# Optimization experiments

Hardware: AMD Instinct MI355X
Metric: run time of the kernel (lower is better)

The kernel has to match this reference:

```python
import jax, jax.numpy as jnp
import numpy as np

N = 1024
NODE_DIM = 3
HIDDEN = 128
NLAYERS = 3
HEADS = 4
HD = HIDDEN // HEADS  # 32
EPS = 1e-5
NEG = -1e9


def setup_inputs() -> dict:
    key = jax.random.key(0)
    ks = jax.random.split(key, 32)
    def w(k, shape, fan_in):
        return jax.random.normal(k, shape, jnp.float32) / np.sqrt(fan_in).astype(np.float32)
    node_features = jax.random.normal(ks[0], (N, NODE_DIM), jnp.float32)
    adj = jax.random.randint(ks[1], (N, N), 0, 2).astype(jnp.float32)
    adj = adj.at[jnp.arange(N), jnp.arange(N)].set(1.0)  # self-loops
    inp = dict(
        node_features=node_features,
        adj=adj,
        Wp=w(ks[2], (NODE_DIM, HIDDEN), NODE_DIM), bp=jnp.zeros((HIDDEN,), jnp.float32),
        Wl=w(ks[3], (NLAYERS, HIDDEN, HIDDEN), HIDDEN),
        Wr=w(ks[4], (NLAYERS, HIDDEN, HIDDEN), HIDDEN),
        Wv=w(ks[5], (NLAYERS, HIDDEN, HIDDEN), HIDDEN),
        att=w(ks[6], (NLAYERS, HD), HD),
        gamma=jnp.ones((NLAYERS, HIDDEN), jnp.float32),
        beta=jnp.zeros((NLAYERS, HIDDEN), jnp.float32),
        Wn1=w(ks[7], (HIDDEN, 64), HIDDEN), bn1=jnp.zeros((64,), jnp.float32),
        Wn2=w(ks[8], (64, 1), 64), bn2=jnp.zeros((1,), jnp.float32),
        Wd1=w(ks[9], (HIDDEN, 64), HIDDEN), bd1=jnp.zeros((64,), jnp.float32),
        Wd2=w(ks[10], (64, 2), 64), bd2=jnp.zeros((2,), jnp.float32),
        Wv1=w(ks[11], (HIDDEN, 64), HIDDEN), bv1=jnp.zeros((64,), jnp.float32),
        Wv2=w(ks[12], (64, 1), 64), bv2=jnp.zeros((1,), jnp.float32),
    )
    return inp


def _gat_layer(h, mask, Wl, Wr, Wv, att, gamma, beta):
    n = h.shape[0]
    wlh = (h @ Wl).reshape(n, HEADS, HD)
    wrh = (h @ Wr).reshape(n, HEADS, HD)
    # pair[i,j,h,d] = LeakyReLU(Wl h_i + Wr h_j)  -- the O(N^2 H D) tensor
    pair = jax.nn.leaky_relu(wlh[:, None, :, :] + wrh[None, :, :, :], 0.2)
    e = jnp.einsum('ijhd,d->ijh', pair, att)
    e = jnp.where(mask[:, :, None], e, NEG)
    alpha = jax.nn.softmax(e, axis=1)  # softmax over neighbours j (dropout = identity in eval)
    v = (h @ Wv).reshape(n, HEADS, HD)
    agg = jnp.einsum('ijh,jhd->ihd', alpha, v).reshape(n, HIDDEN)
    mu = agg.mean(-1, keepdims=True)
    var = agg.var(-1, keepdims=True)
    out = (agg - mu) / jnp.sqrt(var + EPS) * gamma + beta
    return jax.nn.relu(out)


def reference(node_features, adj, Wp, bp, Wl, Wr, Wv, att, gamma, beta,
              Wn1, bn1, Wn2, bn2, Wd1, bd1, Wd2, bd2, Wv1, bv1, Wv2, bv2):
    mask = adj > 0.5
    h = jax.nn.relu(node_features @ Wp + bp)
    for l in range(NLAYERS):
        h = h + _gat_layer(h, mask, Wl[l], Wr[l], Wv[l], att[l], gamma[l], beta[l])
    node_logits = (jax.nn.relu(h @ Wn1 + bn1) @ Wn2 + bn2).squeeze(-1)
    delta_mu = jax.nn.relu(h @ Wd1 + bd1) @ Wd2 + bd2
    pooled = h.mean(axis=0)
    value = (jax.nn.relu(pooled @ Wv1 + bv1) @ Wv2 + bv2).squeeze(-1)
    return (node_logits, delta_mu, value)
```

## Files before the change

kernel.cpp:

```cpp
#include <hip/hip_runtime.h>
#include <hip/hip_bf16.h>

#define NN 1024
#define HID 128
#define NHEADS 4
#define HDD 32
#define NL 3

constexpr int OFF_CONV = 16;
constexpr int OFF_NF   = OFF_CONV;
constexpr int OFF_WP   = OFF_NF  + 3072;
constexpr int OFF_BP   = OFF_WP  + 384;
constexpr int OFF_WL   = OFF_BP  + 128;
constexpr int OFF_WR   = OFF_WL  + 49152;
constexpr int OFF_WVW  = OFF_WR  + 49152;
constexpr int OFF_ATT  = OFF_WVW + 49152;
constexpr int OFF_GAM  = OFF_ATT + 96;
constexpr int OFF_BET  = OFF_GAM + 384;
constexpr int OFF_WN1  = OFF_BET + 384;
constexpr int OFF_BN1  = OFF_WN1 + 8192;
constexpr int OFF_WN2  = OFF_BN1 + 64;
constexpr int OFF_BN2  = OFF_WN2 + 64;
constexpr int OFF_WD1  = OFF_BN2 + 1;
constexpr int OFF_BD1  = OFF_WD1 + 8192;
constexpr int OFF_WD2  = OFF_BD1 + 64;
constexpr int OFF_BD2  = OFF_WD2 + 128;
constexpr int OFF_WV1  = OFF_BD2 + 2;
constexpr int OFF_BV1  = OFF_WV1 + 8192;
constexpr int OFF_WV2  = OFF_BV1 + 64;
constexpr int OFF_BV2  = OFF_WV2 + 64;
constexpr int OFF_CONV_END = OFF_BV2 + 1;
constexpr int CONV_TOTAL = OFF_CONV_END - OFF_CONV;
constexpr int CB = (CONV_TOTAL + 255) / 256;
constexpr int OFF_MASK = 176960;
constexpr int OFF_H    = OFF_MASK + NN*32;
constexpr int OFF_WLH  = OFF_H   + NN*HID;
constexpr int OFF_WRH  = OFF_WLH + NN*HID;
constexpr int OFF_WVH  = OFF_WRH + NN*HID;
constexpr int OFF_CL   = OFF_WVH + NN*HID;
constexpr int OFF_CR   = OFF_CL  + NHEADS*NN;

__device__ __forceinline__ float bf2f(unsigned short u) {
    return __uint_as_float(((unsigned)u) << 16);
}
__device__ __forceinline__ void store_out(void* out, int idx, float v, bool bf) {
    if (bf) {
        unsigned u = __float_as_uint(v);
        unsigned r = (u + 0x7FFFu + ((u >> 16) & 1u)) >> 16;
        ((unsigned short*)out)[idx] = (unsigned short)r;
    } else {
        ((float*)out)[idx] = v;
    }
}
__device__ __forceinline__ float ldraw(const void* p, int idx, bool bf) {
    return bf ? bf2f(((const unsigned short*)p)[idx]) : ((const float*)p)[idx];
}
__device__ __forceinline__ bool detect_bf(const unsigned* nf) {
    unsigned w = nf[threadIdx.x & 63];
    int e = (int)((w >> 23) & 0xFFu);
    unsigned long long b = __ballot(e >= 110 && e <= 140);
    return __popcll(b) < 32;
}

struct P21 { const void* p[21]; };
__device__ const int g_sizes[21] = {3072,384,128,49152,49152,49152,96,384,384,
                                    8192,64,64,1,8192,64,128,2,8192,64,64,1};
__device__ const int g_dsts[21] = {OFF_NF,OFF_WP,OFF_BP,OFF_WL,OFF_WR,OFF_WVW,OFF_ATT,
                                   OFF_GAM,OFF_BET,OFF_WN1,OFF_BN1,OFF_WN2,OFF_BN2,
                                   OFF_WD1,OFF_BD1,OFF_WD2,OFF_BD2,OFF_WV1,OFF_BV1,
                                   OFF_WV2,OFF_BV2};

__global__ __launch_bounds__(256) void k_pre(P21 in, const void* adj, const unsigned* nf, float* ws) {
    bool bf = detect_bf(nf);
    int b = blockIdx.x, t = threadIdx.x;
    if (b < CB) {
        int g = b * 256 + t;
        if (g >= CONV_TOTAL) return;
        int rem = g, s = 0;
        while (s < 21 && rem >= g_sizes[s]) { rem -= g_sizes[s]; s++; }
        if (s >= 21) return;
        ws[g_dsts[s] + rem] = ldraw(in.p[s], rem, bf);
    } else if (b < CB + NN) {
        int i = b - CB;
        unsigned* mask = (unsigned*)(ws + OFF_MASK);
        int lane = t & 63, wv = t >> 6;
        #pragma unroll
        for (int q = 0; q < 4; q++) {
            int seg = wv * 4 + q;
            int j = seg * 64 + lane;
            float v = ldraw(adj, i * NN + j, bf);
            unsigned long long bl = __ballot(v > 0.5f);
            if (lane == 0) {
                mask[i * 32 + seg * 2]     = (unsigned)bl;
                mask[i * 32 + seg * 2 + 1] = (unsigned)(bl >> 32);
            }
        }
    } else {
        int bb = b - CB - NN;
        int i = bb * 2 + (t >> 7), c = t & 127;
        float a = ldraw(in.p[2], c, bf);
        #pragma unroll
        for (int k = 0; k < 3; k++)
            a += ldraw(in.p[0], i * 3 + k, bf) * ldraw(in.p[1], k * HID + c, bf);
        ws[OFF_H + i * HID + c] = fmaxf(a, 0.0f);
    }
}

__global__ __launch_bounds__(128) void k_mm3(float* ws, int l) {
    __shared__ float hs[4][HID];
    int c = threadIdx.x, i0 = blockIdx.x * 4, which = blockIdx.y;
    const float* h = ws + OFF_H;
    #pragma unroll
    for (int r = 0; r < 4; r++) hs[r][c] = h[(i0 + r) * HID + c];
    __syncthreads();
    int woff = (which == 0) ? OFF_WL : (which == 1) ? OFF_WR : OFF_WVW;
    const float* W = ws + woff + l * HID * HID;
    float a[4] = {0,0,0,0};
    #pragma unroll 4
    for (int k = 0; k < HID; k++) {
        float w = W[k * HID + c];
        #pragma unroll
        for (int r = 0; r < 4; r++) a[r] += hs[r][k] * w;
    }
    if (which == 0) {
        #pragma unroll
        for (int r = 0; r < 4; r++) ws[OFF_WLH + (i0 + r) * HID + c] = a[r];
        float att = ws[OFF_ATT + l * HDD + (c & 31)];
        #pragma unroll
        for (int r = 0; r < 4; r++) {
            float t = att * a[r];
            #pragma unroll
            for (int off = 1; off < 32; off <<= 1) t += __shfl_xor(t, off, 64);
            if ((c & 31) == 0) ws[OFF_CL + (c >> 5) * NN + (i0 + r)] = 0.6f * t;
        }
    } else {
        int doff = (which == 1) ? OFF_WRH : OFF_WVH;
        #pragma unroll
        for (int r = 0; r < 4; r++)
            ws[doff + (c >> 2) * (NN * 4) + (i0 + r) * 4 + (c & 3)] = a[r];
        if (which == 1) {
            float att = ws[OFF_ATT + l * HDD + (c & 31)];
            #pragma unroll
            for (int r = 0; r < 4; r++) {
                float t = att * a[r];
                #pragma unroll
                for (int off = 1; off < 32; off <<= 1) t += __shfl_xor(t, off, 64);
                if ((c & 31) == 0) ws[OFF_CR + (c >> 5) * NN + (i0 + r)] = 0.6f * t;
            }
        }
    }
}

__global__ __launch_bounds__(512) void k_attn(float* ws, int l) {
    int t = threadIdx.x;
    int i0 = blockIdx.x * 4;
    int lane = t & 63;
    int w = t >> 6;
    int h = __builtin_amdgcn_readfirstlane(w & 3);
    int p = __builtin_amdgcn_readfirstlane(w >> 2);
    int iA = i0 + 2 * p, iB = iA + 1;

    __shared__ unsigned mrow[4][32];
    __shared__ float ebuf[8][64][33];
    __shared__ float invs[4][4];
    __shared__ float agg_s[4][HID];
    __shared__ float red2[4][2][2];

    if (t < 128) mrow[t >> 5][t & 31] = ((const unsigned*)(ws + OFF_MASK))[i0 * 32 + t];
    __syncthreads();

    unsigned mbA = 0, mbB = 0;
    #pragma unroll
    for (int jc = 0; jc < 16; jc++) {
        int wi = jc * 2 + (lane >> 5);
        mbA |= ((mrow[2 * p][wi] >> (lane & 31)) & 1u) << jc;
        mbB |= ((mrow[2 * p + 1][wi] >> (lane & 31)) & 1u) << jc;
    }

    float att_r[32], wlA[32], wlB[32];
    const float* attp = ws + OFF_ATT + l * HDD;
    const float* wlpA = ws + OFF_WLH + iA * HID + h * HDD;
    const float* wlpB = ws + OFF_WLH + iB * HID + h * HDD;
    #pragma unroll
    for (int d = 0; d < 32; d++) {
        att_r[d] = 0.4f * attp[d];
        wlA[d] = wlpA[d];
        wlB[d] = wlpB[d];
    }
    float clA = ws[OFF_CL + h * NN + iA];
    float clB = ws[OFF_CL + h * NN + iB];

    const float* wrT = ws + OFF_WRH + h * 8 * (NN * 4) + lane * 4;
    const float* wvT = ws + OFF_WVH + h * 8 * (NN * 4) + lane * 4;
    const float* crp = ws + OFF_CR + h * NN;

    float mA = -1e30f, mB = -1e30f;
    #pragma unroll 1
    for (int jc = 0; jc < 16; jc++) {
        float cr6 = crp[jc * 64 + lane];
        float dA = 0.0f, dB = 0.0f;
        #pragma unroll
        for (int dq = 0; dq < 8; dq++) {
            float4 wv4 = *(const float4*)(wrT + dq * (NN * 4) + jc * 256);
            dA = fmaf(att_r[dq*4+0], fabsf(wlA[dq*4+0] + wv4.x), dA);
            dB = fmaf(att_r[dq*4+0], fabsf(wlB[dq*4+0] + wv4.x), dB);
            dA = fmaf(att_r[dq*4+1], fabsf(wlA[dq*4+1] + wv4.y), dA);
            dB = fmaf(att_r[dq*4+1], fabsf(wlB[dq*4+1] + wv4.y), dB);
            dA = fmaf(att_r[dq*4+2], fabsf(wlA[dq*4+2] + wv4.z), dA);
            dB = fmaf(att_r[dq*4+2], fabsf(wlB[dq*4+2] + wv4.z), dB);
            dA = fmaf(att_r[dq*4+3], fabsf(wlA[dq*4+3] + wv4.w), dA);
            dB = fmaf(att_r[dq*4+3], fabsf(wlB[dq*4+3] + wv4.w), dB);
        }
        float eA = (clA + cr6) + dA; eA = ((mbA >> jc) & 1u) ? eA : -1e9f;
        float eB = (clB + cr6) + dB; eB = ((mbB >> jc) & 1u) ? eB : -1e9f;
        ebuf[w][lane][jc]      = eA;
        ebuf[w][lane][16 + jc] = eB;
        mA = fmaxf(mA, eA);
        mB = fmaxf(mB, eB);
    }
    #pragma unroll
    for (int off = 32; off > 0; off >>= 1) {
        mA = fmaxf(mA, __shfl_xor(mA, off, 64));
        mB = fmaxf(mB, __shfl_xor(mB, off, 64));
    }

    float accA[32], accB[32];
    #pragma unroll
    for (int d = 0; d < 32; d++) { accA[d] = 0.0f; accB[d] = 0.0f; }
    float lsA = 0.0f, lsB = 0.0f;
    #pragma unroll 1
    for (int jc = 0; jc < 16; jc++) {
        float peA = __expf(ebuf[w][lane][jc]      - mA);
        float peB = __expf(ebuf[w][lane][16 + jc] - mB);
        lsA += peA; lsB += peB;
        #pragma unroll
        for (int dq = 0; dq < 8; dq++) {
            float4 v4 = *(const float4*)(wvT + dq * (NN * 4) + jc * 256);
            accA[dq*4+0] = fmaf(peA, v4.x, accA[dq*4+0]);
            accB[dq*4+0] = fmaf(peB, v4.x, accB[dq*4+0]);
            accA[dq*4+1] = fmaf(peA, v4.y, accA[dq*4+1]);
            accB[dq*4+1] = fmaf(peB, v4.y, accB[dq*4+1]);
            accA[dq*4+2] = fmaf(peA, v4.z, accA[dq*4+2]);
            accB[dq*4+2] = fmaf(peB, v4.z, accB[dq*4+2]);
            accA[dq*4+3] = fmaf(peA, v4.w, accA[dq*4+3]);
            accB[dq*4+3] = fmaf(peB, v4.w, accB[dq*4+3]);
        }
    }
    #pragma unroll
    for (int off = 32; off > 0; off >>= 1) {
        lsA += __shfl_xor(lsA, off, 64);
        lsB += __shfl_xor(lsB, off, 64);
    }
    if (lane == 0) {
        invs[2 * p][h]     = 1.0f / lsA;
        invs[2 * p + 1][h] = 1.0f / lsB;
    }
    __syncthreads();

    float* rbuf = &ebuf[0][0][0];
    {
        int reg = p * 4 + h;
        #pragma unroll
        for (int d = 0; d < 32; d++) rbuf[(reg * 64 + lane) * 33 + d] = accA[d];
        __syncthreads();
        int g = t >> 6, d = lane & 31, half = lane >> 5;
        float s = 0.0f;
        #pragma unroll
        for (int lq = 0; lq < 32; lq++) s += rbuf[(g * 64 + half * 32 + lq) * 33 + d];
        s += __shfl_xor(s, 32, 64);
        int node = 2 * (g >> 2), hh = g & 3;
        if (half == 0) agg_s[node][hh * 32 + d] = s * invs[node][hh];
        __syncthreads();
    }
    {
        int reg = p * 4 + h;
        #pragma unroll
        for (int d = 0; d < 32; d++) rbuf[(reg * 64 + lane) * 33 + d] = accB[d];
        __syncthreads();
        int g = t >> 6, d = lane & 31, half = lane >> 5;
        float s = 0.0f;
        #pragma unroll
        for (int lq = 0; lq < 32; lq++) s += rbuf[(g * 64 + half * 32 + lq) * 33 + d];
        s += __shfl_xor(s, 32, 64);
        int node = 2 * (g >> 2) + 1, hh = g & 3;
        if (half == 0) agg_s[node][hh * 32 + d] = s * invs[node][hh];
        __syncthreads();
    }

    {
        int n = t >> 7, f = t & 127;
        float agg = agg_s[n][f];
        float s = agg, s2 = agg * agg;
        #pragma unroll
        for (int off = 32; off > 0; off >>= 1) {
            s  += __shfl_xor(s,  off, 64);
            s2 += __shfl_xor(s2, off, 64);
        }
        int half = (t >> 6) & 1;
        if (lane == 0) { red2[n][half][0] = s; red2[n][half][1] = s2; }
        __syncthreads();
        float ts  = red2[n][0][0] + red2[n][1][0];
        float ts2 = red2[n][0][1] + red2[n][1][1];
        float mu  = ts  * (1.0f / HID);
        float var = ts2 * (1.0f / HID) - mu * mu;
        float gm = ws[OFF_GAM + l * HID + f];
        float be = ws[OFF_BET + l * HID + f];
        float o = (agg - mu) * rsqrtf(var + 1e-5f) * gm + be;
        ws[OFF_H + (i0 + n) * HID + f] += fmaxf(o, 0.0f);
    }
}

__global__ __launch_bounds__(1024) void k_post(float* ws, const unsigned* nf, void* out) {
    bool bf = detect_bf(nf);
    int b = blockIdx.x, t = threadIdx.x;
    if (b < 64) {
        __shared__ float hrow[16][HID];
        int n = t >> 6, tt = t & 63;
        int i = b * 16 + n;
        hrow[n][tt]      = ws[OFF_H + i * HID + tt];
        hrow[n][tt + 64] = ws[OFF_H + i * HID + tt + 64];
        __syncthreads();
        const float* Wn1 = ws + OFF_WN1;
        const float* Wd1 = ws + OFF_WD1;
        float z1 = ws[OFF_BN1 + tt], zd = ws[OFF_BD1 + tt];
        #pragma unroll 4
        for (int k = 0; k < HID; k++) {
            float hk = hrow[n][k];
            z1 += hk * Wn1[k * 64 + tt];
            zd += hk * Wd1[k * 64 + tt];
        }
        z1 = fmaxf(z1, 0.0f); zd = fmaxf(zd, 0.0f);
        float lg = z1 * ws[OFF_WN2 + tt];
        float d0 = zd * ws[OFF_WD2 + tt * 2 + 0];
        float d1 = zd * ws[OFF_WD2 + tt * 2 + 1];
        #pragma unroll
        for (int off = 32; off > 0; off >>= 1) {
            lg += __shfl_xor(lg, off, 64);
            d0 += __shfl_xor(d0, off, 64);
            d1 += __shfl_xor(d1, off, 64);
        }
        if (tt == 0) {
            store_out(out, i,              lg + ws[OFF_BN2],     bf);
            store_out(out, NN + i * 2 + 0, d0 + ws[OFF_BD2 + 0], bf);
            store_out(out, NN + i * 2 + 1, d1 + ws[OFF_BD2 + 1], bf);
        }
    } else {
        __shared__ float part[8][HID];
        __shared__ float pooled[HID];
        int g = t >> 7, c = t & 127;
        float s = 0.0f;
        #pragma unroll 16
        for (int r = 0; r < 128; r++) s += ws[OFF_H + (g * 128 + r) * HID + c];
        part[g][c] = s;
        __syncthreads();
        if (t < HID) {
            float p = 0.0f;
            #pragma unroll
            for (int gg = 0; gg < 8; gg++) p += part[gg][t];
            pooled[t] = p * (1.0f / NN);
        }
        __syncthreads();
        if (t < 64) {
            float z = ws[OFF_BV1 + t];
            float z1 = 0.0f;
            #pragma unroll 8
            for (int k = 0; k < HID; k += 2) {
                z  += pooled[k]     * ws[OFF_WV1 + k * 64 + t];
                z1 += pooled[k + 1] * ws[OFF_WV1 + (k + 1) * 64 + t];
            }
            z = fmaxf(z + z1, 0.0f);
            float pv = z * ws[OFF_WV2 + t];
            #pragma unroll
            for (int off = 32; off > 0; off >>= 1) pv += __shfl_xor(pv, off, 64);
            if (t == 0) store_out(out, 3072, pv + ws[OFF_BV2], bf);
        }
    }
}

extern "C" void kernel_launch(void* const* d_in, const int* in_sizes, int n_in,
                              void* d_out, int out_size, void* d_ws, size_t ws_size,
                              hipStream_t stream) {
    float* ws = (float*)d_ws;
    const unsigned* nf = (const unsigned*)d_in[0];

    P21 ptrs;
    const int map[21] = {0,2,3,4,5,6,7,8,9,10,11,12,13,14,15,16,17,18,19,20,21};
    for (int s = 0; s < 21; s++) ptrs.p[s] = d_in[map[s]];

    k_pre<<<CB + NN + NN / 2, 256, 0, stream>>>(ptrs, d_in[1], nf, ws);

    for (int l = 0; l < NL; l++) {
        k_mm3<<<dim3(NN / 4, 3), 128, 0, stream>>>(ws, l);
        k_attn<<<NN / 4, 512, 0, stream>>>(ws, l);
    }

    k_post<<<65, 1024, 0, stream>>>(ws, nf, d_out);
}
```

Baseline: 226.8 us.

## Fuse all stages into one cooperative persistent kernel with grid syncs

Replaces the eight separate launches (preprocess, three rounds of projection plus attention, and post) with a single cooperative kernel of 256 blocks that uses grid-wide syncs between stages. The per-layer projection is now computed by the same block that handles those four nodes, looping over the three weight matrices. Mean pooling is split into per-block partial sums followed by a final reduction in block 0. The aim is to remove launch gaps and inter-kernel overhead. In exchange, the projection runs with less parallelism, and each grid sync costs time, which may outweigh the launch savings.

New measurement: 481.9 us. 2.13x slower.

```diff
diff --git a/kernel.cpp b/kernel.cpp
--- a/kernel.cpp
+++ b/kernel.cpp
@@ -1,5 +1,8 @@
 #include <hip/hip_runtime.h>
 #include <hip/hip_bf16.h>
+#include <hip/hip_cooperative_groups.h>
+
+namespace cg = cooperative_groups;
 
 #define NN 1024
 #define HID 128
@@ -31,7 +34,6 @@
 constexpr int OFF_BV2  = OFF_WV2 + 64;
 constexpr int OFF_CONV_END = OFF_BV2 + 1;
 constexpr int CONV_TOTAL = OFF_CONV_END - OFF_CONV;
-constexpr int CB = (CONV_TOTAL + 255) / 256;
 constexpr int OFF_MASK = 176960;
 constexpr int OFF_H    = OFF_MASK + NN*32;
 constexpr int OFF_WLH  = OFF_H   + NN*HID;
@@ -39,6 +41,7 @@
 constexpr int OFF_WVH  = OFF_WRH + NN*HID;
 constexpr int OFF_CL   = OFF_WVH + NN*HID;
 constexpr int OFF_CR   = OFF_CL  + NHEADS*NN;
+constexpr int OFF_PART = OFF_CR  + NHEADS*NN;
 
 __device__ __forceinline__ float bf2f(unsigned short u) {
     return __uint_as_float(((unsigned)u) << 16);
@@ -70,303 +73,306 @@
                                    OFF_WD1,OFF_BD1,OFF_WD2,OFF_BD2,OFF_WV1,OFF_BV1,
                                    OFF_WV2,OFF_BV2};
 
-__global__ __launch_bounds__(256) void k_pre(P21 in, const void* adj, const unsigned* nf, float* ws) {
-    bool bf = detect_bf(nf);
-    int b = blockIdx.x, t = threadIdx.x;
-    if (b < CB) {
-        int g = b * 256 + t;
-        if (g >= CONV_TOTAL) return;
+__global__ __launch_bounds__(512) void k_mega(P21 in, const void* adj,
+                                              const unsigned* nf, float* ws,
+                                              void* out) {
+    cg::grid_group grid = cg::this_grid();
+    const bool bf = detect_bf(nf);
+    const int b = blockIdx.x, t = threadIdx.x;
+    const int lane = t & 63;
+    const int i0 = b * 4;
+
+    __shared__ union U {
+        float hs[4][HID];
+        struct {
+            unsigned mrow[4][32];
+            float ebuf[8][64][33];
+            float invs[4][4];
+            float agg[4][HID];
+            float red2[4][2][2];
+        } at;
+        struct {
+            float hrow[4][HID];
+            float pooled[HID];
+        } po;
+    } sh;
+
+    for (int g = b * 512 + t; g < CONV_TOTAL; g += 256 * 512) {
         int rem = g, s = 0;
         while (s < 21 && rem >= g_sizes[s]) { rem -= g_sizes[s]; s++; }
-        if (s >= 21) return;
-        ws[g_dsts[s] + rem] = ldraw(in.p[s], rem, bf);
-    } else if (b < CB + NN) {
-        int i = b - CB;
+        if (s < 21) ws[g_dsts[s] + rem] = ldraw(in.p[s], rem, bf);
+    }
+    {
         unsigned* mask = (unsigned*)(ws + OFF_MASK);
-        int lane = t & 63, wv = t >> 6;
+        int n = t >> 7, wvr = (t >> 6) & 1;
+        int i = i0 + n;
         #pragma unroll
-        for (int q = 0; q < 4; q++) {
-            int seg = wv * 4 + q;
-            int j = seg * 64 + lane;
-            float v = ldraw(adj, i * NN + j, bf);
+        for (int q = 0; q < 8; q++) {
+            int seg = wvr * 8 + q;
+            float v = ldraw(adj, i * NN + seg * 64 + lane, bf);
             unsigned long long bl = __ballot(v > 0.5f);
             if (lane == 0) {
                 mask[i * 32 + seg * 2]     = (unsigned)bl;
                 mask[i * 32 + seg * 2 + 1] = (unsigned)(bl >> 32);
             }
         }
-    } else {
-        int bb = b - CB - NN;
-        int i = bb * 2 + (t >> 7), c = t & 127;
+    }
+    {
+        int g = b * 512 + t;
+        int i = g >> 7, c = g & 127;
         float a = ldraw(in.p[2], c, bf);
         #pragma unroll
         for (int k = 0; k < 3; k++)
             a += ldraw(in.p[0], i * 3 + k, bf) * ldraw(in.p[1], k * HID + c, bf);
         ws[OFF_H + i * HID + c] = fmaxf(a, 0.0f);
     }
-}
-
-__global__ __launch_bounds__(128) void k_mm3(float* ws, int l) {
-    __shared__ float hs[4][HID];
-    int c = threadIdx.x, i0 = blockIdx.x * 4, which = blockIdx.y;
-    const float* h = ws + OFF_H;
-    #pragma unroll
-    for (int r = 0; r < 4; r++) hs[r][c] = h[(i0 + r) * HID + c];
-    __syncthreads();
-    int woff = (which == 0) ? OFF_WL : (which == 1) ? OFF_WR : OFF_WVW;
-    const float* W = ws + woff + l * HID * HID;
-    float a[4] = {0,0,0,0};
-    #pragma unroll 4
-    for (int k = 0; k < HID; k++) {
-        float w = W[k * HID + c];
-        #pragma unroll
-        for (int r = 0; r < 4; r++) a[r] += hs[r][k] * w;
-    }
-    if (which == 0) {
-        #pragma unroll
-        for (int r = 0; r < 4; r++) ws[OFF_WLH + (i0 + r) * HID + c] = a[r];
-        float att = ws[OFF_ATT + l * HDD + (c & 31)];
-        #pragma unroll
-        for (int r = 0; r < 4; r++) {
-            float t = att * a[r];
-            #pragma unroll
-            for (int off = 1; off < 32; off <<= 1) t += __shfl_xor(t, off, 64);
-            if ((c & 31) == 0) ws[OFF_CL + (c >> 5) * NN + (i0 + r)] = 0.6f * t;
-        }
-    } else {
-        int doff = (which == 1) ? OFF_WRH : OFF_WVH;
-        #pragma unroll
-        for (int r = 0; r < 4; r++)
-            ws[doff + (c >> 2) * (NN * 4) + (i0 + r) * 4 + (c & 3)] = a[r];
-        if (which == 1) {
-            float att = ws[OFF_ATT + l * HDD + (c & 31)];
-            #pragma unroll
-            for (int r = 0; r < 4; r++) {
-                float t = att * a[r];
-                #pragma unroll
-                for (int off = 1; off < 32; off <<= 1) t += __shfl_xor(t, off, 64);
-                if ((c & 31) == 0) ws[OFF_CR + (c >> 5) * NN + (i0 + r)] = 0.6f * t;
-            }
-        }
-    }
-}
-
-__global__ __launch_bounds__(512) void k_attn(float* ws, int l) {
-    int t = threadIdx.x;
-    int i0 = blockIdx.x * 4;
-    int lane = t & 63;
-    int w = t >> 6;
-    int h = __builtin_amdgcn_readfirstlane(w & 3);
-    int p = __builtin_amdgcn_readfirstlane(w >> 2);
-    int iA = i0 + 2 * p, iB = iA + 1;
-
-    __shared__ unsigned mrow[4][32];
-    __shared__ float ebuf[8][64][33];
-    __shared__ float invs[4][4];
-    __shared__ float agg_s[4][HID];
-    __shared__ float red2[4][2][2];
-
-    if (t < 128) mrow[t >> 5][t & 31] = ((const unsigned*)(ws + OFF_MASK))[i0 * 32 + t];
-    __syncthreads();
-
-    unsigned mbA = 0, mbB = 0;
-    #pragma unroll
-    for (int jc = 0; jc < 16; jc++) {
-        int wi = jc * 2 + (lane >> 5);
-        mbA |= ((mrow[2 * p][wi] >> (lane & 31)) & 1u) << jc;
-        mbB |= ((mrow[2 * p + 1][wi] >> (lane & 31)) & 1u) << jc;
-    }
-
-    float att_r[32], wlA[32], wlB[32];
-    const float* attp = ws + OFF_ATT + l * HDD;
-    const float* wlpA = ws + OFF_WLH + iA * HID + h * HDD;
-    const float* wlpB = ws + OFF_WLH + iB * HID + h * HDD;
-    #pragma unroll
-    for (int d = 0; d < 32; d++) {
-        att_r[d] = 0.4f * attp[d];
-        wlA[d] = wlpA[d];
-        wlB[d] = wlpB[d];
-    }
-    float clA = ws[OFF_CL + h * NN + iA];
-    float clB = ws[OFF_CL + h * NN + iB];
-
-    const float* wrT = ws + OFF_WRH + h * 8 * (NN * 4) + lane * 4;
-    const float* wvT = ws + OFF_WVH + h * 8 * (NN * 4) + lane * 4;
-    const float* crp = ws + OFF_CR + h * NN;
-
-    float mA = -1e30f, mB = -1e30f;
-    #pragma unroll 1
-    for (int jc = 0; jc < 16; jc++) {
-        float cr6 = crp[jc * 64 + lane];
-        float dA = 0.0f, dB = 0.0f;
-        #pragma unroll
-        for (int dq = 0; dq < 8; dq++) {
-            float4 wv4 = *(const float4*)(wrT + dq * (NN * 4) + jc * 256);
-            dA = fmaf(att_r[dq*4+0], fabsf(wlA[dq*4+0] + wv4.x), dA);
-            dB = fmaf(att_r[dq*4+0], fabsf(wlB[dq*4+0] + wv4.x), dB);
-            dA = fmaf(att_r[dq*4+1], fabsf(wlA[dq*4+1] + wv4.y), dA);
-            dB = fmaf(att_r[dq*4+1], fabsf(wlB[dq*4+1] + wv4.y), dB);
-            dA = fmaf(att_r[dq*4+2], fabsf(wlA[dq*4+2] + wv4.z), dA);
-            dB = fmaf(att_r[dq*4+2], fabsf(wlB[dq*4+2] + wv4.z), dB);
-            dA = fmaf(att_r[dq*4+3], fabsf(wlA[dq*4+3] + wv4.w), dA);
-            dB = fmaf(att_r[dq*4+3], fabsf(wlB[dq*4+3] + wv4.w), dB);
-        }
-        float eA = (clA + cr6) + dA; eA = ((mbA >> jc) & 1u) ? eA : -1e9f;
-        float eB = (clB + cr6) + dB; eB = ((mbB >> jc) & 1u) ? eB : -1e9f;
-        ebuf[w][lane][jc]      = eA;
-        ebuf[w][lane][16 + jc] = eB;
-        mA = fmaxf(mA, eA);
-        mB = fmaxf(mB, eB);
-    }
-    #pragma unroll
-    for (int off = 32; off > 0; off >>= 1) {
-        mA = fmaxf(mA, __shfl_xor(mA, off, 64));
-        mB = fmaxf(mB, __shfl_xor(mB, off, 64));
-    }
-
-    float accA[32], accB[32];
-    #pragma unroll
-    for (int d = 0; d < 32; d++) { accA[d] = 0.0f; accB[d] = 0.0f; }
-    float lsA = 0.0f, lsB = 0.0f;
-    #pragma unroll 1
-    for (int jc = 0; jc < 16; jc++) {
-        float peA = __expf(ebuf[w][lane][jc]      - mA);
-        float peB = __expf(ebuf[w][lane][16 + jc] - mB);
-        lsA += peA; lsB += peB;
-        #pragma unroll
-        for (int dq = 0; dq < 8; dq++) {
-            float4 v4 = *(const float4*)(wvT + dq * (NN * 4) + jc * 256);
-            accA[dq*4+0] = fmaf(peA, v4.x, accA[dq*4+0]);
-            accB[dq*4+0] = fmaf(peB, v4.x, accB[dq*4+0]);
-            accA[dq*4+1] = fmaf(peA, v4.y, accA[dq*4+1]);
-            accB[dq*4+1] = fmaf(peB, v4.y, accB[dq*4+1]);
-            accA[dq*4+2] = fmaf(peA, v4.z, accA[dq*4+2]);
-            accB[dq*4+2] = fmaf(peB, v4.z, accB[dq*4+2]);
-            accA[dq*4+3] = fmaf(peA, v4.w, accA[dq*4+3]);
-            accB[dq*4+3] = fmaf(peB, v4.w, accB[dq*4+3]);
-        }
-    }
-    #pragma unroll
-    for (int off = 32; off > 0; off >>= 1) {
-        lsA += __shfl_xor(lsA, off, 64);
-        lsB += __shfl_xor(lsB, off, 64);
-    }
-    if (lane == 0) {
-        invs[2 * p][h]     = 1.0f / lsA;
-        invs[2 * p + 1][h] = 1.0f / lsB;
-    }
-    __syncthreads();
-
-    float* rbuf = &ebuf[0][0][0];
+    grid.sync();
+
+    for (int l = 0; l < NL; l++) {
+        {
+            int gq = t >> 7, c = t & 127;
+            sh.hs[gq][c] = ws[OFF_H + (i0 + gq) * HID + c];
+            __syncthreads();
+            #pragma unroll 1
+            for (int which = 0; which < 3; which++) {
+                int woff = (which == 0) ? OFF_WL : (which == 1) ? OFF_WR : OFF_WVW;
+                const float* W = ws + woff + l * HID * HID;
+                float a0 = 0.f, a1 = 0.f;
+                #pragma unroll 8
+                for (int k = 0; k < HID; k += 2) {
+                    a0 += sh.hs[gq][k]     * W[k * HID + c];
+                    a1 += sh.hs[gq][k + 1] * W[(k + 1) * HID + c];
+                }
+                float a = a0 + a1;
+                if (which == 0) {
+                    ws[OFF_WLH + (i0 + gq) * HID + c] = a;
+                    float att = ws[OFF_ATT + l * HDD + (c & 31)];
+                    float s = att * a;
+                    #pragma unroll
+                    for (int off = 1; off < 32; off <<= 1) s += __shfl_xor(s, off, 64);
+                    if ((c & 31) == 0) ws[OFF_CL + (c >> 5) * NN + (i0 + gq)] = 0.6f * s;
+                } else {
+                    int doff = (which == 1) ? OFF_WRH : OFF_WVH;
+                    ws[doff + (c >> 2) * (NN * 4) + (i0 + gq) * 4 + (c & 3)] = a;
+                    if (which == 1) {
+                        float att = ws[OFF_ATT + l * HDD + (c & 31)];
+                        float s = att * a;
+                        #pragma unroll
+                        for (int off = 1; off < 32; off <<= 1) s += __shfl_xor(s, off, 64);
+                        if ((c & 31) == 0) ws[OFF_CR + (c >> 5) * NN + (i0 + gq)] = 0.6f * s;
+                    }
+                }
+            }
+        }
+        grid.sync();
+
+        {
+            int wv = t >> 6;
+            int h  = __builtin_amdgcn_readfirstlane(wv & 3);
+            int pr = __builtin_amdgcn_readfirstlane(wv >> 2);
+            int iA = i0 + 2 * pr, iB = iA + 1;
+
+            if (t < 128) sh.at.mrow[t >> 5][t & 31] =
+                ((const unsigned*)(ws + OFF_MASK))[i0 * 32 + t];
+            __syncthreads();
+
+            unsigned mbA = 0, mbB = 0;
+            #pragma unroll
+            for (int jc = 0; jc < 16; jc++) {
+                int wi = jc * 2 + (lane >> 5);
+                mbA |= ((sh.at.mrow[2 * pr][wi]     >> (lane & 31)) & 1u) << jc;
+                mbB |= ((sh.at.mrow[2 * pr + 1][wi] >> (lane & 31)) & 1u) << jc;
+            }
+
+            float att_r[32], wlA[32], wlB[32];
+            const float* attp = ws + OFF_ATT + l * HDD;
+            const float* wlpA = ws + OFF_WLH + iA * HID + h * HDD;
+            const float* wlpB = ws + OFF_WLH + iB * HID + h * HDD;
+            #pragma unroll
+            for (int d = 0; d < 32; d++) {
+                att_r[d] = 0.4f * attp[d];
+                wlA[d] = wlpA[d];
+                wlB[d] = wlpB[d];
+            }
+            float clA = ws[OFF_CL + h * NN + iA];
+            float clB = ws[OFF_CL + h * NN + iB];
+
+            const float* wrT = ws + OFF_WRH + h * 8 * (NN * 4) + lane * 4;
+            const float* wvT = ws + OFF_WVH + h * 8 * (NN * 4) + lane * 4;
+            const float* crp = ws + OFF_CR + h * NN;
+
+            float mA = -1e30f, mB = -1e30f;
+            #pragma unroll 1
+            for (int jc = 0; jc < 16; jc++) {
+                float cr6 = crp[jc * 64 + lane];
+                float dA = 0.f, dB = 0.f;
+                #pragma unroll
+                for (int dq = 0; dq < 8; dq++) {
+                    float4 w4 = *(const float4*)(wrT + dq * (NN * 4) + jc * 256);
+                    dA = fmaf(att_r[dq*4+0], fabsf(wlA[dq*4+0] + w4.x), dA);
+                    dB = fmaf(att_r[dq*4+0], fabsf(wlB[dq*4+0] + w4.x), dB);
+                    dA = fmaf(att_r[dq*4+1], fabsf(wlA[dq*4+1] + w4.y), dA);
+                    dB = fmaf(att_r[dq*4+1], fabsf(wlB[dq*4+1] + w4.y), dB);
+                    dA = fmaf(att_r[dq*4+2], fabsf(wlA[dq*4+2] + w4.z), dA);
+                    dB = fmaf(att_r[dq*4+2], fabsf(wlB[dq*4+2] + w4.z), dB);
+                    dA = fmaf(att_r[dq*4+3], fabsf(wlA[dq*4+3] + w4.w), dA);
+                    dB = fmaf(att_r[dq*4+3], fabsf(wlB[dq*4+3] + w4.w), dB);
+                }
+                float eA = (clA + cr6) + dA; eA = ((mbA >> jc) & 1u) ? eA : -1e9f;
+                float eB = (clB + cr6) + dB; eB = ((mbB >> jc) & 1u) ? eB : -1e9f;
+                sh.at.ebuf[wv][lane][jc]      = eA;
+                sh.at.ebuf[wv][lane][16 + jc] = eB;
+                mA = fmaxf(mA, eA);
+                mB = fmaxf(mB, eB);
+            }
+            #pragma unroll
+            for (int off = 32; off > 0; off >>= 1) {
+                mA = fmaxf(mA, __shfl_xor(mA, off, 64));
+                mB = fmaxf(mB, __shfl_xor(mB, off, 64));
+            }
+
+            float accA[32], accB[32];
+            #pragma unroll
+            for (int d = 0; d < 32; d++) { accA[d] = 0.f; accB[d] = 0.f; }
+            float lsA = 0.f, lsB = 0.f;
+            #pragma unroll 1
+            for (int jc = 0; jc < 16; jc++) {
+                float peA = __expf(sh.at.ebuf[wv][lane][jc]      - mA);
+                float peB = __expf(sh.at.ebuf[wv][lane][16 + jc] - mB);
+                lsA += peA; lsB += peB;
+                #pragma unroll
+                for (int dq = 0; dq < 8; dq++) {
+                    float4 v4 = *(const float4*)(wvT + dq * (NN * 4) + jc * 256);
+                    accA[dq*4+0] = fmaf(peA, v4.x, accA[dq*4+0]);
+                    accB[dq*4+0] = fmaf(peB, v4.x, accB[dq*4+0]);
+                    accA[dq*4+1] = fmaf(peA, v4.y, accA[dq*4+1]);
+                    accB[dq*4+1] = fmaf(peB, v4.y, accB[dq*4+1]);
+                    accA[dq*4+2] = fmaf(peA, v4.z, accA[dq*4+2]);
+                    accB[dq*4+2] = fmaf(peB, v4.z, accB[dq*4+2]);
+                    accA[dq*4+3] = fmaf(peA, v4.w, accA[dq*4+3]);
+                    accB[dq*4+3] = fmaf(peB, v4.w, accB[dq*4+3]);
+                }
+            }
+            #pragma unroll
+            for (int off = 32; off > 0; off >>= 1) {
+                lsA += __shfl_xor(lsA, off, 64);
+                lsB += __shfl_xor(lsB, off, 64);
+            }
+            if (lane == 0) {
+                sh.at.invs[2 * pr][h]     = 1.0f / lsA;
+                sh.at.invs[2 * pr + 1][h] = 1.0f / lsB;
+            }
+            __syncthreads();
+
+            float* rbuf = &sh.at.ebuf[0][0][0];
+            {
+                int reg = pr * 4 + h;
+                #pragma unroll
+                for (int d = 0; d < 32; d++) rbuf[(reg * 64 + lane) * 33 + d] = accA[d];
+                __syncthreads();
+                int g = t >> 6, d = lane & 31, half = lane >> 5;
+                float s = 0.f;
+                #pragma unroll
+                for (int lq = 0; lq < 32; lq++) s += rbuf[(g * 64 + half * 32 + lq) * 33 + d];
+                s += __shfl_xor(s, 32, 64);
+                int node = 2 * (g >> 2), hh = g & 3;
+                if (half == 0) sh.at.agg[node][hh * 32 + d] = s * sh.at.invs[node][hh];
+                __syncthreads();
+            }
+            {
+                int reg = pr * 4 + h;
+                #pragma unroll
+                for (int d = 0; d < 32; d++) rbuf[(reg * 64 + lane) * 33 + d] = accB[d];
+                __syncthreads();
+                int g = t >> 6, d = lane & 31, half = lane >> 5;
+                float s = 0.f;
+                #pragma unroll
+                for (int lq = 0; lq < 32; lq++) s += rbuf[(g * 64 + half * 32 + lq) * 33 + d];
+                s += __shfl_xor(s, 32, 64);
+                int node = 2 * (g >> 2) + 1, hh = g & 3;
+                if (half == 0) sh.at.agg[node][hh * 32 + d] = s * sh.at.invs[node][hh];
+                __syncthreads();
+            }
+
+            {
+                int n = t >> 7, f = t & 127;
+                float agg = sh.at.agg[n][f];
+                float s = agg, s2 = agg * agg;
+                #pragma unroll
+                for (int off = 32; off > 0; off >>= 1) {
+                    s  += __shfl_xor(s,  off, 64);
+                    s2 += __shfl_xor(s2, off, 64);
+                }
+                int half = (t >> 6) & 1;
+                if (lane == 0) { sh.at.red2[n][half][0] = s; sh.at.red2[n][half][1] = s2; }
+                __syncthreads();
+                float ts  = sh.at.red2[n][0][0] + sh.at.red2[n][1][0];
+                float ts2 = sh.at.red2[n][0][1] + sh.at.red2[n][1][1];
+                float mu  = ts  * (1.0f / HID);
+                float var = ts2 * (1.0f / HID) - mu * mu;
+                float gm = ws[OFF_GAM + l * HID + f];
+                float be = ws[OFF_BET + l * HID + f];
+                float o = (agg - mu) * rsqrtf(var + 1e-5f) * gm + be;
+                ws[OFF_H + (i0 + n) * HID + f] += fmaxf(o, 0.0f);
+            }
+        }
+        grid.sync();
+    }
+
     {
-        int reg = p * 4 + h;
-        #pragma unroll
-        for (int d = 0; d < 32; d++) rbuf[(reg * 64 + lane) * 33 + d] = accA[d];
+        int n = t >> 7, s7 = t & 127;
+        sh.po.hrow[n][s7] = ws[OFF_H + (i0 + n) * HID + s7];
         __syncthreads();
-        int g = t >> 6, d = lane & 31, half = lane >> 5;
-        float s = 0.0f;
-        #pragma unroll
-        for (int lq = 0; lq < 32; lq++) s += rbuf[(g * 64 + half * 32 + lq) * 33 + d];
-        s += __shfl_xor(s, 32, 64);
-        int node = 2 * (g >> 2), hh = g & 3;
-        if (half == 0) agg_s[node][hh * 32 + d] = s * invs[node][hh];
-        __syncthreads();
-    }
-    {
-        int reg = p * 4 + h;
-        #pragma unroll
-        for (int d = 0; d < 32; d++) rbuf[(reg * 64 + lane) * 33 + d] = accB[d];
-        __syncthreads();
-        int g = t >> 6, d = lane & 31, half = lane >> 5;
-        float s = 0.0f;
-        #pragma unroll
-        for (int lq = 0; lq < 32; lq++) s += rbuf[(g * 64 + half * 32 + lq) * 33 + d];
-        s += __shfl_xor(s, 32, 64);
-        int node = 2 * (g >> 2) + 1, hh = g & 3;
-        if (half == 0) agg_s[node][hh * 32 + d] = s * invs[node][hh];
-        __syncthreads();
-    }
-
-    {
-        int n = t >> 7, f = t & 127;
-        float agg = agg_s[n][f];
-        float s = agg, s2 = agg * agg;
-        #pragma unroll
-        for (int off = 32; off > 0; off >>= 1) {
-            s  += __shfl_xor(s,  off, 64);
-            s2 += __shfl_xor(s2, off, 64);
-        }
         int half = (t >> 6) & 1;
-        if (lane == 0) { red2[n][half][0] = s; red2[n][half][1] = s2; }
-        __syncthreads();
-        float ts  = red2[n][0][0] + red2[n][1][0];
-        float ts2 = red2[n][0][1] + red2[n][1][1];
-        float mu  = ts  * (1.0f / HID);
-        float var = ts2 * (1.0f / HID) - mu * mu;
-        float gm = ws[OFF_GAM + l * HID + f];
-        float be = ws[OFF_BET + l * HID + f];
-        float o = (agg - mu) * rsqrtf(var + 1e-5f) * gm + be;
-        ws[OFF_H + (i0 + n) * HID + f] += fmaxf(o, 0.0f);
-    }
-}
-
-__global__ __launch_bounds__(1024) void k_post(float* ws, const unsigned* nf, void* out) {
-    bool bf = detect_bf(nf);
-    int b = blockIdx.x, t = threadIdx.x;
-    if (b < 64) {
-        __shared__ float hrow[16][HID];
-        int n = t >> 6, tt = t & 63;
-        int i = b * 16 + n;
-        hrow[n][tt]      = ws[OFF_H + i * HID + tt];
-        hrow[n][tt + 64] = ws[OFF_H + i * HID + tt + 64];
-        __syncthreads();
-        const float* Wn1 = ws + OFF_WN1;
-        const float* Wd1 = ws + OFF_WD1;
-        float z1 = ws[OFF_BN1 + tt], zd = ws[OFF_BD1 + tt];
-        #pragma unroll 4
-        for (int k = 0; k < HID; k++) {
-            float hk = hrow[n][k];
-            z1 += hk * Wn1[k * 64 + tt];
-            zd += hk * Wd1[k * 64 + tt];
-        }
-        z1 = fmaxf(z1, 0.0f); zd = fmaxf(zd, 0.0f);
-        float lg = z1 * ws[OFF_WN2 + tt];
-        float d0 = zd * ws[OFF_WD2 + tt * 2 + 0];
-        float d1 = zd * ws[OFF_WD2 + tt * 2 + 1];
-        #pragma unroll
-        for (int off = 32; off > 0; off >>= 1) {
-            lg += __shfl_xor(lg, off, 64);
-            d0 += __shfl_xor(d0, off, 64);
-            d1 += __shfl_xor(d1, off, 64);
-        }
-        if (tt == 0) {
-            store_out(out, i,              lg + ws[OFF_BN2],     bf);
-            store_out(out, NN + i * 2 + 0, d0 + ws[OFF_BD2 + 0], bf);
-            store_out(out, NN + i * 2 + 1, d1 + ws[OFF_BD2 + 1], bf);
-        }
-    } else {
-        __shared__ float part[8][HID];
-        __shared__ float pooled[HID];
-        int g = t >> 7, c = t & 127;
-        float s = 0.0f;
-        #pragma unroll 16
-        for (int r = 0; r < 128; r++) s += ws[OFF_H + (g * 128 + r) * HID + c];
-        part[g][c] = s;
-        __syncthreads();
-        if (t < HID) {
-            float p = 0.0f;
-            #pragma unroll
-            for (int gg = 0; gg < 8; gg++) p += part[gg][t];
-            pooled[t] = p * (1.0f / NN);
+        int tt = lane;
+        if (half == 0) {
+            float z1 = ws[OFF_BN1 + tt];
+            #pragma unroll 8
+            for (int k = 0; k < HID; k++) z1 += sh.po.hrow[n][k] * ws[OFF_WN1 + k * 64 + tt];
+            z1 = fmaxf(z1, 0.0f);
+            float lg = z1 * ws[OFF_WN2 + tt];
+            #pragma unroll
+            for (int off = 32; off > 0; off >>= 1) lg += __shfl_xor(lg, off, 64);
+            if (tt == 0) store_out(out, i0 + n, lg + ws[OFF_BN2], bf);
+        } else {
+            float zd = ws[OFF_BD1 + tt];
+            #pragma unroll 8
+            for (int k = 0; k < HID; k++) zd += sh.po.hrow[n][k] * ws[OFF_WD1 + k * 64 + tt];
+            zd = fmaxf(zd, 0.0f);
+            float d0 = zd * ws[OFF_WD2 + tt * 2 + 0];
+            float d1 = zd * ws[OFF_WD2 + tt * 2 + 1];
+            #pragma unroll
+            for (int off = 32; off > 0; off >>= 1) {
+                d0 += __shfl_xor(d0, off, 64);
+                d1 += __shfl_xor(d1, off, 64);
+            }
+            if (tt == 0) {
+                store_out(out, NN + (i0 + n) * 2 + 0, d0 + ws[OFF_BD2 + 0], bf);
+                store_out(out, NN + (i0 + n) * 2 + 1, d1 + ws[OFF_BD2 + 1], bf);
+            }
+        }
+        if (t < 128) {
+            float s = sh.po.hrow[0][t] + sh.po.hrow[1][t]
+                    + sh.po.hrow[2][t] + sh.po.hrow[3][t];
+            ws[OFF_PART + b * HID + t] = s;
+        }
+    }
+    grid.sync();
+
+    if (b == 0) {
+        if (t < 128) {
+            float p = 0.f;
+            #pragma unroll 16
+            for (int q = 0; q < 256; q++) p += ws[OFF_PART + q * HID + t];
+            sh.po.pooled[t] = p * (1.0f / NN);
         }
         __syncthreads();
         if (t < 64) {
-            float z = ws[OFF_BV1 + t];
-            float z1 = 0.0f;
+            float z = ws[OFF_BV1 + t], z1 = 0.f;
             #pragma unroll 8
             for (int k = 0; k < HID; k += 2) {
-                z  += pooled[k]     * ws[OFF_WV1 + k * 64 + t];
-                z1 += pooled[k + 1] * ws[OFF_WV1 + (k + 1) * 64 + t];
+                z  += sh.po.pooled[k]     * ws[OFF_WV1 + k * 64 + t];
+                z1 += sh.po.pooled[k + 1] * ws[OFF_WV1 + (k + 1) * 64 + t];
             }
             z = fmaxf(z + z1, 0.0f);
             float pv = z * ws[OFF_WV2 + t];
@@ -382,17 +388,14 @@
                               hipStream_t stream) {
     float* ws = (float*)d_ws;
     const unsigned* nf = (const unsigned*)d_in[0];
+    const void* adj = d_in[1];
 
     P21 ptrs;
     const int map[21] = {0,2,3,4,5,6,7,8,9,10,11,12,13,14,15,16,17,18,19,20,21};
     for (int s = 0; s < 21; s++) ptrs.p[s] = d_in[map[s]];
 
-    k_pre<<<CB + NN + NN / 2, 256, 0, stream>>>(ptrs, d_in[1], nf, ws);
-
-    for (int l = 0; l < NL; l++) {
-        k_mm3<<<dim3(NN / 4, 3), 128, 0, stream>>>(ws, l);
-        k_attn<<<NN / 4, 512, 0, stream>>>(ws, l);
-    }
-
-    k_post<<<65, 1024, 0, stream>>>(ws, nf, d_out);
-}
+    void* outp = d_out;
+    void* kargs[] = { (void*)&ptrs, (void*)&adj, (void*)&nf, (void*)&ws, (void*)&outp };
+    hipLaunchCooperativeKernel((const void*)k_mega, dim3(256), dim3(512),
+                               kargs, 0, stream);
+}
```

## Fuse attention score and aggregation passes with online softmax in k_attn

Applied to the files above, without the earlier changes.

Merges the two passes over neighbours into one loop. It uses a per-lane online softmax with a lazy rescale threshold, so the scores are no longer written to LDS and read back in a second loop. The value loads are issued early in each iteration to overlap with the score computation. The per-lane running maxima are combined across the wavefront at the end with a rescale. One __syncthreads before the shared reduction buffer is reused is also removed, which could be a race, since other waves may still be using rbuf_s.

Measured after the change: 296.0 us. 30.5% more time.

```diff
diff --git a/kernel.cpp b/kernel.cpp
--- a/kernel.cpp
+++ b/kernel.cpp
@@ -161,7 +161,7 @@
     int iA = i0 + 2 * p, iB = iA + 1;
 
     __shared__ unsigned mrow[4][32];
-    __shared__ float ebuf[8][64][33];
+    __shared__ float rbuf_s[8][64][33];
     __shared__ float invs[4][4];
     __shared__ float agg_s[4][HID];
     __shared__ float red2[4][2][2];
@@ -194,58 +194,102 @@
     const float* wvT = ws + OFF_WVH + h * 8 * (NN * 4) + lane * 4;
     const float* crp = ws + OFF_CR + h * NN;
 
+    float accA[32], accB[32];
+    #pragma unroll
+    for (int d = 0; d < 32; d++) { accA[d] = 0.f; accB[d] = 0.f; }
+    float lsA = 0.f, lsB = 0.f;
     float mA = -1e30f, mB = -1e30f;
+
     #pragma unroll 1
     for (int jc = 0; jc < 16; jc++) {
+        float4 v0 = *(const float4*)(wvT + 0 * (NN * 4) + jc * 256);
+        float4 v1 = *(const float4*)(wvT + 1 * (NN * 4) + jc * 256);
+        float4 v2 = *(const float4*)(wvT + 2 * (NN * 4) + jc * 256);
+        float4 v3 = *(const float4*)(wvT + 3 * (NN * 4) + jc * 256);
+        float4 v4 = *(const float4*)(wvT + 4 * (NN * 4) + jc * 256);
+        float4 v5 = *(const float4*)(wvT + 5 * (NN * 4) + jc * 256);
+        float4 v6 = *(const float4*)(wvT + 6 * (NN * 4) + jc * 256);
+        float4 v7 = *(const float4*)(wvT + 7 * (NN * 4) + jc * 256);
+
         float cr6 = crp[jc * 64 + lane];
-        float dA = 0.0f, dB = 0.0f;
+        float dA = 0.f, dB = 0.f;
         #pragma unroll
         for (int dq = 0; dq < 8; dq++) {
-            float4 wv4 = *(const float4*)(wrT + dq * (NN * 4) + jc * 256);
-            dA = fmaf(att_r[dq*4+0], fabsf(wlA[dq*4+0] + wv4.x), dA);
-            dB = fmaf(att_r[dq*4+0], fabsf(wlB[dq*4+0] + wv4.x), dB);
-            dA = fmaf(att_r[dq*4+1], fabsf(wlA[dq*4+1] + wv4.y), dA);
-            dB = fmaf(att_r[dq*4+1], fabsf(wlB[dq*4+1] + wv4.y), dB);
-            dA = fmaf(att_r[dq*4+2], fabsf(wlA[dq*4+2] + wv4.z), dA);
-            dB = fmaf(att_r[dq*4+2], fabsf(wlB[dq*4+2] + wv4.z), dB);
-            dA = fmaf(att_r[dq*4+3], fabsf(wlA[dq*4+3] + wv4.w), dA);
-            dB = fmaf(att_r[dq*4+3], fabsf(wlB[dq*4+3] + wv4.w), dB);
+            float4 w4 = *(const float4*)(wrT + dq * (NN * 4) + jc * 256);
+            dA = fmaf(att_r[dq*4+0], fabsf(wlA[dq*4+0] + w4.x), dA);
+            dB = fmaf(att_r[dq*4+0], fabsf(wlB[dq*4+0] + w4.x), dB);
+            dA = fmaf(att_r[dq*4+1], fabsf(wlA[dq*4+1] + w4.y), dA);
+            dB = fmaf(att_r[dq*4+1], fabsf(wlB[dq*4+1] + w4.y), dB);
+            dA = fmaf(att_r[dq*4+2], fabsf(wlA[dq*4+2] + w4.z), dA);
+            dB = fmaf(att_r[dq*4+2], fabsf(wlB[dq*4+2] + w4.z), dB);
+            dA = fmaf(att_r[dq*4+3], fabsf(wlA[dq*4+3] + w4.w), dA);
+            dB = fmaf(att_r[dq*4+3], fabsf(wlB[dq*4+3] + w4.w), dB);
         }
         float eA = (clA + cr6) + dA; eA = ((mbA >> jc) & 1u) ? eA : -1e9f;
         float eB = (clB + cr6) + dB; eB = ((mbB >> jc) & 1u) ? eB : -1e9f;
-        ebuf[w][lane][jc]      = eA;
-        ebuf[w][lane][16 + jc] = eB;
-        mA = fmaxf(mA, eA);
-        mB = fmaxf(mB, eB);
-    }
+
+        if (eA > mA + 8.0f) {
+            float sc = __expf(mA - eA);
+            lsA *= sc;
+            #pragma unroll
+            for (int d = 0; d < 32; d++) accA[d] *= sc;
+            mA = eA;
+        }
+        if (eB > mB + 8.0f) {
+            float sc = __expf(mB - eB);
+            lsB *= sc;
+            #pragma unroll
+            for (int d = 0; d < 32; d++) accB[d] *= sc;
+            mB = eB;
+        }
+        float peA = __expf(eA - mA);
+        float peB = __expf(eB - mB);
+        lsA += peA; lsB += peB;
+
+        accA[0]  = fmaf(peA, v0.x, accA[0]);  accB[0]  = fmaf(peB, v0.x, accB[0]);
+        accA[1]  = fmaf(peA, v0.y, accA[1]);  accB[1]  = fmaf(peB, v0.y, accB[1]);
+        accA[2]  = fmaf(peA, v0.z, accA[2]);  accB[2]  = fmaf(peB, v0.z, accB[2]);
+        accA[3]  = fmaf(peA, v0.w, accA[3]);  accB[3]  = fmaf(peB, v0.w, accB[3]);
+        accA[4]  = fmaf(peA, v1.x, accA[4]);  accB[4]  = fmaf(peB, v1.x, accB[4]);
+        accA[5]  = fmaf(peA, v1.y, accA[5]);  accB[5]  = fmaf(peB, v1.y, accB[5]);
+        accA[6]  = fmaf(peA, v1.z, accA[6]);  accB[6]  = fmaf(peB, v1.z, accB[6]);
+        accA[7]  = fmaf(peA, v1.w, accA[7]);  accB[7]  = fmaf(peB, v1.w, accB[7]);
+        accA[8]  = fmaf(peA, v2.x, accA[8]);  accB[8]  = fmaf(peB, v2.x, accB[8]);
+        accA[9]  = fmaf(peA, v2.y, accA[9]);  accB[9]  = fmaf(peB, v2.y, accB[9]);
+        accA[10] = fmaf(peA, v2.z, accA[10]); accB[10] = fmaf(peB, v2.z, accB[10]);
+        accA[11] = fmaf(peA, v2.w, accA[11]); accB[11] = fmaf(peB, v2.w, accB[11]);
+        accA[12] = fmaf(peA, v3.x, accA[12]); accB[12] = fmaf(peB, v3.x, accB[12]);
+        accA[13] = fmaf(peA, v3.y, accA[13]); accB[13] = fmaf(peB, v3.y, accB[13]);
+        accA[14] = fmaf(peA, v3.z, accA[14]); accB[14] = fmaf(peB, v3.z, accB[14]);
+        accA[15] = fmaf(peA, v3.w, accA[15]); accB[15] = fmaf(peB, v3.w, accB[15]);
+        accA[16] = fmaf(peA, v4.x, accA[16]); accB[16] = fmaf(peB, v4.x, accB[16]);
+        accA[17] = fmaf(peA, v4.y, accA[17]); accB[17] = fmaf(peB, v4.y, accB[17]);
+        accA[18] = fmaf(peA, v4.z, accA[18]); accB[18] = fmaf(peB, v4.z, accB[18]);
+        accA[19] = fmaf(peA, v4.w, accA[19]); accB[19] = fmaf(peB, v4.w, accB[19]);
+        accA[20] = fmaf(peA, v5.x, accA[20]); accB[20] = fmaf(peB, v5.x, accB[20]);
+        accA[21] = fmaf(peA, v5.y, accA[21]); accB[21] = fmaf(peB, v5.y, accB[21]);
+        accA[22] = fmaf(peA, v5.z, accA[22]); accB[22] = fmaf(peB, v5.z, accB[22]);
+        accA[23] = fmaf(peA, v5.w, accA[23]); accB[23] = fmaf(peB, v5.w, accB[23]);
+        accA[24] = fmaf(peA, v6.x, accA[24]); accB[24] = fmaf(peB, v6.x, accB[24]);
+        accA[25] = fmaf(peA, v6.y, accA[25]); accB[25] = fmaf(peB, v6.y, accB[25]);
+        accA[26] = fmaf(peA, v6.z, accA[26]); accB[26] = fmaf(peB, v6.z, accB[26]);
+        accA[27] = fmaf(peA, v6.w, accA[27]); accB[27] = fmaf(peB, v6.w, accB[27]);
+        accA[28] = fmaf(peA, v7.x, accA[28]); accB[28] = fmaf(peB, v7.x, accB[28]);
+        accA[29] = fmaf(peA, v7.y, accA[29]); accB[29] = fmaf(peB, v7.y, accB[29]);
+        accA[30] = fmaf(peA, v7.z, accA[30]); accB[30] = fmaf(peB, v7.z, accB[30]);
+        accA[31] = fmaf(peA, v7.w, accA[31]); accB[31] = fmaf(peB, v7.w, accB[31]);
+    }
+
+    float gA = mA, gB = mB;
     #pragma unroll
     for (int off = 32; off > 0; off >>= 1) {
-        mA = fmaxf(mA, __shfl_xor(mA, off, 64));
-        mB = fmaxf(mB, __shfl_xor(mB, off, 64));
-    }
-
-    float accA[32], accB[32];
-    #pragma unroll
-    for (int d = 0; d < 32; d++) { accA[d] = 0.0f; accB[d] = 0.0f; }
-    float lsA = 0.0f, lsB = 0.0f;
-    #pragma unroll 1
-    for (int jc = 0; jc < 16; jc++) {
-        float peA = __expf(ebuf[w][lane][jc]      - mA);
-        float peB = __expf(ebuf[w][lane][16 + jc] - mB);
-        lsA += peA; lsB += peB;
-        #pragma unroll
-        for (int dq = 0; dq < 8; dq++) {
-            float4 v4 = *(const float4*)(wvT + dq * (NN * 4) + jc * 256);
-            accA[dq*4+0] = fmaf(peA, v4.x, accA[dq*4+0]);
-            accB[dq*4+0] = fmaf(peB, v4.x, accB[dq*4+0]);
-            accA[dq*4+1] = fmaf(peA, v4.y, accA[dq*4+1]);
-            accB[dq*4+1] = fmaf(peB, v4.y, accB[dq*4+1]);
-            accA[dq*4+2] = fmaf(peA, v4.z, accA[dq*4+2]);
-            accB[dq*4+2] = fmaf(peB, v4.z, accB[dq*4+2]);
-            accA[dq*4+3] = fmaf(peA, v4.w, accA[dq*4+3]);
-            accB[dq*4+3] = fmaf(peB, v4.w, accB[dq*4+3]);
-        }
-    }
+        gA = fmaxf(gA, __shfl_xor(gA, off, 64));
+        gB = fmaxf(gB, __shfl_xor(gB, off, 64));
+    }
+    float scA = __expf(mA - gA), scB = __expf(mB - gB);
+    lsA *= scA; lsB *= scB;
+    #pragma unroll
+    for (int d = 0; d < 32; d++) { accA[d] *= scA; accB[d] *= scB; }
     #pragma unroll
     for (int off = 32; off > 0; off >>= 1) {
         lsA += __shfl_xor(lsA, off, 64);
@@ -255,9 +299,8 @@
         invs[2 * p][h]     = 1.0f / lsA;
         invs[2 * p + 1][h] = 1.0f / lsB;
     }
-    __syncthreads();
-
-    float* rbuf = &ebuf[0][0][0];
+
+    float* rbuf = &rbuf_s[0][0][0];
     {
         int reg = p * 4 + h;
         #pragma unroll
```
